# Kernel optimization log

Hardware: AMD Instinct MI355X
Metric: run time of the kernel (lower is better)

## Reference

```python
import jax, jax.numpy as jnp
import numpy as np
import math

H, KVH, D = 15, 5, 64  # heads, kv heads, head_dim
ROPE_BASE = 10000.0
NEG = -1e9


def _rope_cos_sin(position_ids):
    # position_ids: [B, S] int -> cos/sin [B, 1, S, D]
    inv_freq = 1.0 / (ROPE_BASE ** (jnp.arange(0, D, 2, dtype=jnp.float32) / D))  # [D/2]
    freqs = position_ids.astype(jnp.float32)[..., None] * inv_freq  # [B, S, D/2]
    emb = jnp.concatenate([freqs, freqs], axis=-1)  # [B, S, D]
    return jnp.cos(emb)[:, None], jnp.sin(emb)[:, None]


def _rotate_half(x):
    x1, x2 = x[..., : D // 2], x[..., D // 2 :]
    return jnp.concatenate([-x2, x1], axis=-1)


def setup_inputs() -> dict:
    key = jax.random.key(0)
    ks = jax.random.split(key, 5)
    B, S, E = 1, 4096, 960
    hidden_states = jax.random.normal(ks[0], (B, S, E), dtype=jnp.float32)
    Wq = jax.random.normal(ks[1], (E, E), dtype=jnp.float32) * 0.02
    Wk = jax.random.normal(ks[2], (KVH * D, E), dtype=jnp.float32) * 0.02
    Wv = jax.random.normal(ks[3], (KVH * D, E), dtype=jnp.float32) * 0.02
    Wo = jax.random.normal(ks[4], (E, E), dtype=jnp.float32) * 0.02
    causal = jnp.tril(jnp.ones((S, S), dtype=bool))
    attention_mask = jnp.where(causal, 0.0, NEG).astype(jnp.float32)[None, None]  # [1,1,S,S]
    position_ids = jnp.arange(S, dtype=jnp.int64 if jax.config.jax_enable_x64 else jnp.int32)[None]
    return {
        "hidden_states": hidden_states,
        "Wq": Wq,
        "Wk": Wk,
        "Wv": Wv,
        "Wo": Wo,
        "attention_mask": attention_mask,
        "position_ids": position_ids,
    }


def reference(hidden_states, Wq, Wk, Wv, Wo, attention_mask, position_ids):
    B, S, E = hidden_states.shape
    groups = H // KVH
    # projections (bias-free Linear: x @ W.T)
    q = (hidden_states @ Wq.T).reshape(B, S, H, D).transpose(0, 2, 1, 3)      # [B,H,S,D]
    k = (hidden_states @ Wk.T).reshape(B, S, KVH, D).transpose(0, 2, 1, 3)    # [B,KVH,S,D]
    v = (hidden_states @ Wv.T).reshape(B, S, KVH, D).transpose(0, 2, 1, 3)    # [B,KVH,S,D]
    cos, sin = _rope_cos_sin(position_ids)  # [B,1,S,D]
    q = q * cos + _rotate_half(q) * sin
    k = k * cos + _rotate_half(k) * sin
    # GQA: repeat_interleave over the head axis
    k = jnp.repeat(k, groups, axis=1)  # [B,H,S,D]
    v = jnp.repeat(v, groups, axis=1)  # [B,H,S,D]
    scores = jnp.einsum("bhqd,bhkd->bhqk", q, k) / math.sqrt(D) + attention_mask
    probs = jax.nn.softmax(scores.astype(jnp.float32), axis=-1).astype(q.dtype)
    out = jnp.einsum("bhqk,bhkd->bhqd", probs, v)  # [B,H,S,D]
    out = out.transpose(0, 2, 1, 3).reshape(B, S, E)
    return out @ Wo.T
```

## Files before the change

kernel.cpp:

```cpp
#include <hip/hip_runtime.h>
#include <hip/hip_bf16.h>

typedef __hip_bfloat16 bf16;
typedef short bf16x8 __attribute__((ext_vector_type(8)));
typedef short bf16x4 __attribute__((ext_vector_type(4)));
typedef float f32x4 __attribute__((ext_vector_type(4)));

static constexpr int S_LEN = 4096;
static constexpr int EMB   = 960;
static constexpr int NH    = 15;
static constexpr int NKVH  = 5;
static constexpr int KV_E  = NKVH * 64;

__device__ __forceinline__ float scrub(float x, float lim) {
  return fminf(fmaxf(x, -lim), lim);
}

__device__ __forceinline__ short f2bf(float x) {
  bf16 h = __float2bfloat16(x);
  short s;
  __builtin_memcpy(&s, &h, 2);
  return s;
}

__device__ __forceinline__ void stage16(const bf16* g, bf16* l) {
  __builtin_amdgcn_global_load_lds(
      (const __attribute__((address_space(1))) void*)g,
      (__attribute__((address_space(3))) void*)l, 16, 0, 0);
}

__global__ void cvt5_kernel(const float* s0, const float* s1, const float* s2,
                            const float* s3, const float* s4,
                            bf16* d0, bf16* d1, bf16* d2, bf16* d3, bf16* d4,
                            int e0, int e1, int e2, int e3, int e4) {
  int i = blockIdx.x * blockDim.x + threadIdx.x;
  const float* s;
  bf16* d;
  int base;
  if (i < e0)      { s = s0; d = d0; base = 0;  }
  else if (i < e1) { s = s1; d = d1; base = e0; }
  else if (i < e2) { s = s2; d = d2; base = e1; }
  else if (i < e3) { s = s3; d = d3; base = e2; }
  else if (i < e4) { s = s4; d = d4; base = e3; }
  else return;
  int k = i - base;
  const float4* sp = (const float4*)s + (size_t)k * 2;
  float4 a = sp[0], b = sp[1];
  bf16x8 r;
  r[0] = f2bf(a.x); r[1] = f2bf(a.y); r[2] = f2bf(a.z); r[3] = f2bf(a.w);
  r[4] = f2bf(b.x); r[5] = f2bf(b.y); r[6] = f2bf(b.z); r[7] = f2bf(b.w);
  *(bf16x8*)((short*)d + (size_t)k * 8) = r;
}

template <typename EPI>
__device__ __forceinline__ void gemm_core64(
    const bf16* __restrict__ A, const bf16* __restrict__ W,
    int m0, int n0, int K, bf16* At, bf16* Bt, EPI&& epilogue) {
  const int lane = threadIdx.x & 63;
  const int wv   = threadIdx.x >> 6;
  const int quad = lane >> 4;
  const int c16  = lane & 15;
  const int rsub = lane >> 3;
  const int gch  = (lane & 7) ^ rsub;
  const int rm   = c16 & 7;
  const int NIT  = K / 64;

  auto stage = [&](int b, int k0) {
#pragma unroll
    for (int t = 0; t < 2; t++) {
      int i = wv * 2 + t;
      int r = i * 8 + rsub;
      stage16(A + (unsigned)((m0 + r) * K + k0 + gch * 8),
              At + b * 4096 + i * 512);
      stage16(W + (unsigned)((n0 + r) * K + k0 + gch * 8),
              Bt + b * 4096 + i * 512);
    }
  };

  f32x4 acc[4];
#pragma unroll
  for (int j = 0; j < 4; j++) acc[j] = (f32x4){0.f, 0.f, 0.f, 0.f};

  stage(0, 0);
  stage(1, 64);
  int ib = 0;

  for (int it = 0; it < NIT; ++it) {
    if (it + 1 < NIT) {
      asm volatile("s_waitcnt vmcnt(4)" ::: "memory");
    } else {
      asm volatile("s_waitcnt vmcnt(0)" ::: "memory");
    }
    __builtin_amdgcn_s_barrier();
    __builtin_amdgcn_sched_barrier(0);
    if (it + 2 < NIT) {
      int sb = ib + 2; if (sb >= 3) sb -= 3;
      stage(sb, (it + 2) * 64);
    }
    const char* ab = (const char*)(At + ib * 4096);
    const char* bb = (const char*)(Bt + ib * 4096);
    const int ra = wv * 16 + c16;
#pragma unroll
    for (int kh = 0; kh < 2; kh++) {
      const int ko = ((kh * 4 + quad) ^ rm) * 16;
      bf16x8 af = *(const bf16x8*)(ab + ra * 128 + ko);
#pragma unroll
      for (int j = 0; j < 4; j++) {
        bf16x8 bfr = *(const bf16x8*)(bb + (j * 16 + c16) * 128 + ko);
        acc[j] = __builtin_amdgcn_mfma_f32_16x16x32_bf16(af, bfr,
                                                         acc[j], 0, 0, 0);
      }
    }
    ib = (ib + 1 == 3) ? 0 : ib + 1;
  }
  epilogue(acc, m0, n0, wv, quad, c16);
}

__global__ __launch_bounds__(256) void gemm_qkv_kernel(
    const bf16* __restrict__ A, const bf16* __restrict__ Wcat,
    bf16* __restrict__ Qb, bf16* __restrict__ Kbf, bf16* __restrict__ VTb,
    const int* __restrict__ pos, int M, int K) {
  __shared__ __align__(16) bf16 At[3][64 * 64];
  __shared__ __align__(16) bf16 Bt[3][64 * 64];
  const int m0 = blockIdx.x * 64;
  const int n0 = blockIdx.y * 64;
  gemm_core64(A, Wcat, m0, n0, K, At[0], Bt[0],
              [&](f32x4 (&acc)[4], int m0_, int n0_, int wv, int quad,
                  int c16) {
                if (n0_ < 1280) {
                  const bool isQ = (n0_ < 960);
                  bf16* dst = isQ ? Qb : Kbf;
                  const int stride = isQ ? EMB : KV_E;
                  const int cbase = isQ ? n0_ : (n0_ - 960);
                  const float scale = isQ ? 0.18033688011112042f : 1.0f;
#pragma unroll
                  for (int j = 0; j < 2; j++) {
                    int d = j * 16 + c16;
                    float invf = expf(-0.28782313662425572f * (float)d);
                    int row0 = m0_ + wv * 16 + quad * 4;
#pragma unroll
                    for (int r = 0; r < 4; r++) {
                      int row = row0 + r;
                      float th = (float)pos[row] * invf;
                      float sf, cf;
                      sincosf(th, &sf, &cf);
                      float x = acc[j][r];
                      float y = acc[j + 2][r];
                      size_t base = (size_t)row * stride + cbase + j * 16 + c16;
                      dst[base] =
                          __float2bfloat16(scrub((x * cf - y * sf) * scale, 3e4f));
                      dst[base + 32] =
                          __float2bfloat16(scrub((y * cf + x * sf) * scale, 3e4f));
                    }
                  }
                } else {
#pragma unroll
                  for (int j = 0; j < 4; j++) {
                    int d = n0_ + j * 16 + c16 - 1280;
                    bf16x4 v;
#pragma unroll
                    for (int r = 0; r < 4; r++)
                      v[r] = f2bf(scrub(acc[j][r], 3e4f));
                    int nl = (quad + 4 * (wv >> 1)) * 8 + (wv & 1) * 4;
                    *(bf16x4*)((short*)VTb + (size_t)d * S_LEN + m0_ + nl) = v;
                  }
                }
              });
}

__global__ __launch_bounds__(256) void gemm_out_kernel(
    const bf16* __restrict__ A, const bf16* __restrict__ W,
    float* __restrict__ C, int M, int N, int K) {
  __shared__ __align__(16) bf16 At[3][64 * 64];
  __shared__ __align__(16) bf16 Bt[3][64 * 64];
  const int m0 = blockIdx.x * 64;
  const int n0 = blockIdx.y * 64;
  gemm_core64(A, W, m0, n0, K, At[0], Bt[0],
              [&](f32x4 (&acc)[4], int m0_, int n0_, int wv, int quad,
                  int c16) {
                int row0 = m0_ + wv * 16 + quad * 4;
#pragma unroll
                for (int j = 0; j < 4; j++) {
                  int col = n0_ + j * 16 + c16;
#pragma unroll
                  for (int r = 0; r < 4; r++)
                    C[(size_t)(row0 + r) * EMB + col] =
                        scrub(acc[j][r], 3e4f);
                }
              });
}

__global__ __launch_bounds__(256, 2) void flash_kernel(
    const bf16* Q, const bf16* __restrict__ Kb,
    const bf16* __restrict__ VT, bf16* O) {
  __shared__ __align__(16) bf16 Kt[2][128 * 64];
  __shared__ __align__(16) bf16 Vt[2][64 * 128];

  const int bx = blockIdx.x;
  const int lane = threadIdx.x & 63;
  const int wv   = threadIdx.x >> 6;
  const int quad = lane >> 4;
  const int c16  = lane & 15;
  const int h    = blockIdx.y;
  const int kvh  = h / 3;

  const int rsub = lane >> 3;
  const int gch  = (lane & 7) ^ rsub;
  const int vr4  = lane >> 4;
  const int vhf  = (lane >> 3) & 1;
  const int rm   = c16 & 7;
  const int ko0  = (quad ^ rm) * 16;

  bf16x4 ones4;
#pragma unroll
  for (int j = 0; j < 4; j++) ones4[j] = (short)0x3F80;

  auto stage = [&](int b, int t) {
    const int kbase = t * 128;
#pragma unroll
    for (int tt = 0; tt < 4; tt++) {
      int i = wv * 4 + tt;
      int r = i * 8 + rsub;
      stage16(Kb + (unsigned)((kbase + r) * KV_E + kvh * 64 + gch * 8),
              &Kt[b][i * 512]);
    }
#pragma unroll
    for (int tt = 0; tt < 4; tt++) {
      int i = wv * 4 + tt;
      int row = i * 4 + vr4;
      int g = (lane & 7) ^ (row & 7);
      stage16(VT + (unsigned)((kvh * 64 + row) * S_LEN + kbase + vhf * 64 +
                              g * 8),
              &Vt[b][i * 512]);
    }
  };

  auto run_strip = [&](int xq) {
    const int qw    = xq * 64 + wv * 16;
    const int qcol  = qw + c16;
    const int itend = (xq + 2) >> 1;

    __syncthreads();

    const bf16* qrow = Q + (size_t)qcol * EMB + h * 64 + quad * 8;
    const bf16x8 aq0 = *(const bf16x8*)qrow;
    const bf16x8 aq1 = *(const bf16x8*)(qrow + 32);

    f32x4 o[4];
#pragma unroll
    for (int n = 0; n < 4; n++) o[n] = (f32x4){0.f, 0.f, 0.f, 0.f};
    f32x4 os = (f32x4){0.f, 0.f, 0.f, 0.f};

    stage(0, 0);

    for (int it = 0; it < itend; ++it) {
      __syncthreads();
      if (it + 1 < itend) stage((it + 1) & 1, it + 1);

      const int kbase = it * 128;
      const char* kb = (const char*)&Kt[it & 1][0];
      const char* vb = (const char*)&Vt[it & 1][0];
      const bool masked = (it == itend - 1);

      bf16x4 pp[8];
      __builtin_amdgcn_s_setprio(1);
#pragma unroll
      for (int cc = 0; cc < 8; cc++) {
        int r = cc * 16 + c16;
        bf16x8 b0 = *(const bf16x8*)(kb + r * 128 + ko0);
        bf16x8 b1 = *(const bf16x8*)(kb + r * 128 + (ko0 ^ 64));
        f32x4 s = (f32x4){0.f, 0.f, 0.f, 0.f};
        s = __builtin_amdgcn_mfma_f32_16x16x32_bf16(b0, aq0, s, 0, 0, 0);
        s = __builtin_amdgcn_mfma_f32_16x16x32_bf16(b1, aq1, s, 0, 0, 0);
#pragma unroll
        for (int r4 = 0; r4 < 4; r4++) {
          float p = exp2f(s[r4]);
          if (masked) {
            int kc = kbase + cc * 16 + quad * 4 + r4;
            p = (kc <= qcol) ? p : 0.f;
          }
          pp[cc][r4] = f2bf(p);
        }
      }

#pragma unroll
      for (int cc = 0; cc < 8; cc++)
        os = __builtin_amdgcn_mfma_f32_16x16x16bf16_1k(ones4, pp[cc], os,
                                                       0, 0, 0);

#pragma unroll
      for (int n = 0; n < 4; n++) {
        const char* vrow = vb + (n * 16 + c16) * 256;
        bf16x8 va = *(const bf16x8*)(vrow + ko0);
        bf16x8 vb2 = *(const bf16x8*)(vrow + (ko0 ^ 64));
        bf16x8 vc = *(const bf16x8*)(vrow + 128 + ko0);
        bf16x8 vd = *(const bf16x8*)(vrow + 128 + (ko0 ^ 64));
        bf16x4 a0 = __builtin_shufflevector(va, va, 0, 1, 2, 3);
        bf16x4 a1 = __builtin_shufflevector(va, va, 4, 5, 6, 7);
        bf16x4 a2 = __builtin_shufflevector(vb2, vb2, 0, 1, 2, 3);
        bf16x4 a3 = __builtin_shufflevector(vb2, vb2, 4, 5, 6, 7);
        bf16x4 a4 = __builtin_shufflevector(vc, vc, 0, 1, 2, 3);
        bf16x4 a5 = __builtin_shufflevector(vc, vc, 4, 5, 6, 7);
        bf16x4 a6 = __builtin_shufflevector(vd, vd, 0, 1, 2, 3);
        bf16x4 a7 = __builtin_shufflevector(vd, vd, 4, 5, 6, 7);
        o[n] = __builtin_amdgcn_mfma_f32_16x16x16bf16_1k(a0, pp[0], o[n], 0, 0, 0);
        o[n] = __builtin_amdgcn_mfma_f32_16x16x16bf16_1k(a1, pp[1], o[n], 0, 0, 0);
        o[n] = __builtin_amdgcn_mfma_f32_16x16x16bf16_1k(a2, pp[2], o[n], 0, 0, 0);
        o[n] = __builtin_amdgcn_mfma_f32_16x16x16bf16_1k(a3, pp[3], o[n], 0, 0, 0);
        o[n] = __builtin_amdgcn_mfma_f32_16x16x16bf16_1k(a4, pp[4], o[n], 0, 0, 0);
        o[n] = __builtin_amdgcn_mfma_f32_16x16x16bf16_1k(a5, pp[5], o[n], 0, 0, 0);
        o[n] = __builtin_amdgcn_mfma_f32_16x16x16bf16_1k(a6, pp[6], o[n], 0, 0, 0);
        o[n] = __builtin_amdgcn_mfma_f32_16x16x16bf16_1k(a7, pp[7], o[n], 0, 0, 0);
      }
      __builtin_amdgcn_s_setprio(0);
    }

    const float inv = 1.0f / fmaxf(os[0], 1e-20f);
#pragma unroll
    for (int n = 0; n < 4; n++) {
      bf16x4 w;
#pragma unroll
      for (int r = 0; r < 4; r++)
        w[r] = f2bf(scrub(o[n][r] * inv, 1e4f));
      *(bf16x4*)((short*)O + (size_t)qcol * EMB + h * 64 + n * 16 +
                 quad * 4) = w;
    }
  };

  run_strip(63 - bx);
  run_strip(bx);
}

extern "C" void kernel_launch(void* const* d_in, const int* in_sizes, int n_in,
                              void* d_out, int out_size, void* d_ws, size_t ws_size,
                              hipStream_t stream) {
  const float* hs = (const float*)d_in[0];
  const float* Wq = (const float*)d_in[1];
  const float* Wk = (const float*)d_in[2];
  const float* Wv = (const float*)d_in[3];
  const float* Wo = (const float*)d_in[4];
  const int* pos = (const int*)d_in[6];
  float* out = (float*)d_out;

  char* wsb = (char*)d_ws;
  size_t regA = ((size_t)S_LEN * EMB + (size_t)S_LEN * NH) * sizeof(float);
  bf16* hsb = (bf16*)wsb;
  bf16* Qb  = (bf16*)(wsb + regA);
  bf16* Kbf = Qb + (size_t)S_LEN * EMB;
  bf16* VTb = Kbf + (size_t)S_LEN * KV_E;
  bf16* Wqb = VTb + (size_t)S_LEN * KV_E;
  bf16* Wkb = Wqb + (size_t)EMB * EMB;
  bf16* Wvb = Wkb + (size_t)KV_E * EMB;
  bf16* Wob = Wqb + (size_t)1664 * EMB;

  {
    int e0 = (S_LEN * EMB) / 8;
    int e1 = e0 + (EMB * EMB) / 8;
    int e2 = e1 + (KV_E * EMB) / 8;
    int e3 = e2 + (KV_E * EMB) / 8;
    int e4 = e3 + (EMB * EMB) / 8;
    cvt5_kernel<<<(e4 + 255) / 256, 256, 0, stream>>>(
        hs, Wq, Wk, Wv, Wo, hsb, Wqb, Wkb, Wvb, Wob, e0, e1, e2, e3, e4);
  }

  gemm_qkv_kernel<<<dim3(S_LEN / 64, 25), 256, 0, stream>>>(
      hsb, Wqb, Qb, Kbf, VTb, pos, S_LEN, EMB);

  flash_kernel<<<dim3(32, NH), 256, 0, stream>>>(Qb, Kbf, VTb, Qb);

  gemm_out_kernel<<<dim3(S_LEN / 64, 15), 256, 0, stream>>>(
      Qb, Wob, out, S_LEN, EMB, EMB);
}
```

Measured before the change: 244.0 us.

## Split flash attention KV tile across two wave groups with LDS reduction

Doubles the flash kernel block to 512 threads. Each 128-key tile is split into two 64-key halves handled by separate groups of four waves, and the partial outputs and denominators are combined through shared memory at the end of each query strip. This halves the per-wave serial MFMA chain and increases waves per CU, which is meant to hide latency better given only 480 blocks. The cost is an extra LDS reduction plus two barriers per strip, and the higher launch-bounds occupancy target may limit registers.

```diff
diff --git a/kernel.cpp b/kernel.cpp
--- a/kernel.cpp
+++ b/kernel.cpp
@@ -190,7 +190,7 @@
               });
 }
 
-__global__ __launch_bounds__(256, 2) void flash_kernel(
+__global__ __launch_bounds__(512, 4) void flash_kernel(
     const bf16* Q, const bf16* __restrict__ Kb,
     const bf16* __restrict__ VT, bf16* O) {
   __shared__ __align__(16) bf16 Kt[2][128 * 64];
@@ -199,6 +199,8 @@
   const int bx = blockIdx.x;
   const int lane = threadIdx.x & 63;
   const int wv   = threadIdx.x >> 6;
+  const int kg   = wv >> 2;
+  const int wq   = wv & 3;
   const int quad = lane >> 4;
   const int c16  = lane & 15;
   const int h    = blockIdx.y;
@@ -218,15 +220,15 @@
   auto stage = [&](int b, int t) {
     const int kbase = t * 128;
 #pragma unroll
-    for (int tt = 0; tt < 4; tt++) {
-      int i = wv * 4 + tt;
+    for (int tt = 0; tt < 2; tt++) {
+      int i = wv * 2 + tt;
       int r = i * 8 + rsub;
       stage16(Kb + (unsigned)((kbase + r) * KV_E + kvh * 64 + gch * 8),
               &Kt[b][i * 512]);
     }
 #pragma unroll
-    for (int tt = 0; tt < 4; tt++) {
-      int i = wv * 4 + tt;
+    for (int tt = 0; tt < 2; tt++) {
+      int i = wv * 2 + tt;
       int row = i * 4 + vr4;
       int g = (lane & 7) ^ (row & 7);
       stage16(VT + (unsigned)((kvh * 64 + row) * S_LEN + kbase + vhf * 64 +
@@ -236,7 +238,7 @@
   };
 
   auto run_strip = [&](int xq) {
-    const int qw    = xq * 64 + wv * 16;
+    const int qw    = xq * 64 + wq * 16;
     const int qcol  = qw + c16;
     const int itend = (xq + 2) >> 1;
 
@@ -257,16 +259,16 @@
       __syncthreads();
       if (it + 1 < itend) stage((it + 1) & 1, it + 1);
 
-      const int kbase = it * 128;
+      const int kbase = it * 128 + kg * 64;
       const char* kb = (const char*)&Kt[it & 1][0];
       const char* vb = (const char*)&Vt[it & 1][0];
       const bool masked = (it == itend - 1);
 
-      bf16x4 pp[8];
+      bf16x4 pp[4];
       __builtin_amdgcn_s_setprio(1);
 #pragma unroll
-      for (int cc = 0; cc < 8; cc++) {
-        int r = cc * 16 + c16;
+      for (int cc = 0; cc < 4; cc++) {
+        int r = kg * 64 + cc * 16 + c16;
         bf16x8 b0 = *(const bf16x8*)(kb + r * 128 + ko0);
         bf16x8 b1 = *(const bf16x8*)(kb + r * 128 + (ko0 ^ 64));
         f32x4 s = (f32x4){0.f, 0.f, 0.f, 0.f};
@@ -284,46 +286,57 @@
       }
 
 #pragma unroll
-      for (int cc = 0; cc < 8; cc++)
+      for (int cc = 0; cc < 4; cc++)
         os = __builtin_amdgcn_mfma_f32_16x16x16bf16_1k(ones4, pp[cc], os,
                                                        0, 0, 0);
 
 #pragma unroll
       for (int n = 0; n < 4; n++) {
-        const char* vrow = vb + (n * 16 + c16) * 256;
+        const char* vrow = vb + (n * 16 + c16) * 256 + kg * 128;
         bf16x8 va = *(const bf16x8*)(vrow + ko0);
-        bf16x8 vb2 = *(const bf16x8*)(vrow + (ko0 ^ 64));
-        bf16x8 vc = *(const bf16x8*)(vrow + 128 + ko0);
-        bf16x8 vd = *(const bf16x8*)(vrow + 128 + (ko0 ^ 64));
+        bf16x8 vc = *(const bf16x8*)(vrow + (ko0 ^ 64));
         bf16x4 a0 = __builtin_shufflevector(va, va, 0, 1, 2, 3);
         bf16x4 a1 = __builtin_shufflevector(va, va, 4, 5, 6, 7);
-        bf16x4 a2 = __builtin_shufflevector(vb2, vb2, 0, 1, 2, 3);
-        bf16x4 a3 = __builtin_shufflevector(vb2, vb2, 4, 5, 6, 7);
-        bf16x4 a4 = __builtin_shufflevector(vc, vc, 0, 1, 2, 3);
-        bf16x4 a5 = __builtin_shufflevector(vc, vc, 4, 5, 6, 7);
-        bf16x4 a6 = __builtin_shufflevector(vd, vd, 0, 1, 2, 3);
-        bf16x4 a7 = __builtin_shufflevector(vd, vd, 4, 5, 6, 7);
-        o[n] = __builtin_amdgcn_mfma_f32_16x16x16bf16_1k(a0, pp[0], o[n], 0, 0, 0);
-        o[n] = __builtin_amdgcn_mfma_f32_16x16x16bf16_1k(a1, pp[1], o[n], 0, 0, 0);
-        o[n] = __builtin_amdgcn_mfma_f32_16x16x16bf16_1k(a2, pp[2], o[n], 0, 0, 0);
-        o[n] = __builtin_amdgcn_mfma_f32_16x16x16bf16_1k(a3, pp[3], o[n], 0, 0, 0);
-        o[n] = __builtin_amdgcn_mfma_f32_16x16x16bf16_1k(a4, pp[4], o[n], 0, 0, 0);
-        o[n] = __builtin_amdgcn_mfma_f32_16x16x16bf16_1k(a5, pp[5], o[n], 0, 0, 0);
-        o[n] = __builtin_amdgcn_mfma_f32_16x16x16bf16_1k(a6, pp[6], o[n], 0, 0, 0);
-        o[n] = __builtin_amdgcn_mfma_f32_16x16x16bf16_1k(a7, pp[7], o[n], 0, 0, 0);
+        bf16x4 a2 = __builtin_shufflevector(vc, vc, 0, 1, 2, 3);
+        bf16x4 a3 = __builtin_shufflevector(vc, vc, 4, 5, 6, 7);
+        o[n] = __builtin_amdgcn_mfma_f32_16x16x16bf16_1k(a0, pp[0], o[n],
+                                                         0, 0, 0);
+        o[n] = __builtin_amdgcn_mfma_f32_16x16x16bf16_1k(a1, pp[1], o[n],
+                                                         0, 0, 0);
+        o[n] = __builtin_amdgcn_mfma_f32_16x16x16bf16_1k(a2, pp[2], o[n],
+                                                         0, 0, 0);
+        o[n] = __builtin_amdgcn_mfma_f32_16x16x16bf16_1k(a3, pp[3], o[n],
+                                                         0, 0, 0);
       }
       __builtin_amdgcn_s_setprio(0);
     }
 
-    const float inv = 1.0f / fmaxf(os[0], 1e-20f);
-#pragma unroll
-    for (int n = 0; n < 4; n++) {
-      bf16x4 w;
-#pragma unroll
-      for (int r = 0; r < 4; r++)
-        w[r] = f2bf(scrub(o[n][r] * inv, 1e4f));
-      *(bf16x4*)((short*)O + (size_t)qcol * EMB + h * 64 + n * 16 +
-                 quad * 4) = w;
+    __syncthreads();
+    float* slot = (float*)&Kt[0][0] + ((wq * 64 + lane) * 17);
+    if (kg == 1) {
+#pragma unroll
+      for (int n = 0; n < 4; n++)
+#pragma unroll
+        for (int r = 0; r < 4; r++) slot[n * 4 + r] = o[n][r];
+      slot[16] = os[0];
+    }
+    __syncthreads();
+    if (kg == 0) {
+#pragma unroll
+      for (int n = 0; n < 4; n++)
+#pragma unroll
+        for (int r = 0; r < 4; r++) o[n][r] += slot[n * 4 + r];
+      const float den = os[0] + slot[16];
+      const float inv = 1.0f / fmaxf(den, 1e-20f);
+#pragma unroll
+      for (int n = 0; n < 4; n++) {
+        bf16x4 w;
+#pragma unroll
+        for (int r = 0; r < 4; r++)
+          w[r] = f2bf(scrub(o[n][r] * inv, 1e4f));
+        *(bf16x4*)((short*)O + (size_t)qcol * EMB + h * 64 + n * 16 +
+                   quad * 4) = w;
+      }
     }
   };
 
@@ -366,7 +379,7 @@
   gemm_qkv_kernel<<<dim3(S_LEN / 64, 25), 256, 0, stream>>>(
       hsb, Wqb, Qb, Kbf, VTb, pos, S_LEN, EMB);
 
-  flash_kernel<<<dim3(32, NH), 256, 0, stream>>>(Qb, Kbf, VTb, Qb);
+  flash_kernel<<<dim3(32, NH), 512, 0, stream>>>(Qb, Kbf, VTb, Qb);
 
   gemm_out_kernel<<<dim3(S_LEN / 64, 15), 256, 0, stream>>>(
       Qb, Wob, out, S_LEN, EMB, EMB);
```

New measurement: 237.7 us. 2.5% less time.
